# Optimization experiments

Measured on AMD Instinct MI355X. Metric: run time of the kernel, lower is better.

## Reference

```python
import jax, jax.numpy as jnp
import numpy as np

D_MODEL = 2048
NUM_HEADS = 16
NUM_GROUPS = 4
HEAD_DIM = D_MODEL // NUM_HEADS
ROPE_THETA = 10000.0


def apply_rope(x):
    # x: [B, S, H, Dh]; positions = arange(S); interleaved-pair rotary
    B, S, H, Dh = x.shape
    inv_freq = 1.0 / (ROPE_THETA ** (jnp.arange(0, Dh, 2, dtype=jnp.float32) / Dh))  # [Dh/2]
    pos = jnp.arange(S, dtype=jnp.float32)
    ang = pos[:, None] * inv_freq[None, :]            # [S, Dh/2]
    cos = jnp.cos(ang)[None, :, None, :]              # [1, S, 1, Dh/2]
    sin = jnp.sin(ang)[None, :, None, :]
    x1 = x[..., 0::2]
    x2 = x[..., 1::2]
    r1 = x1 * cos - x2 * sin
    r2 = x1 * sin + x2 * cos
    return jnp.stack([r1, r2], axis=-1).reshape(B, S, H, Dh)


def setup_inputs() -> dict:
    key = jax.random.key(0)
    kx, kq, kk, kv, ko = jax.random.split(key, 5)
    B, S = 4, 4096
    x = jax.random.normal(kx, (B, S, D_MODEL), dtype=jnp.float32)
    init = 0.02
    Wq = jax.random.normal(kq, (D_MODEL, D_MODEL), dtype=jnp.float32) * init
    Wk = jax.random.normal(kk, (D_MODEL, D_MODEL), dtype=jnp.float32) * init
    Wv = jax.random.normal(kv, (D_MODEL, D_MODEL), dtype=jnp.float32) * init
    Wo = jax.random.normal(ko, (D_MODEL, D_MODEL), dtype=jnp.float32) * init
    return {"x": x, "Wq": Wq, "Wk": Wk, "Wv": Wv, "Wo": Wo}


def reference(x, Wq, Wk, Wv, Wo):
    B, S, _ = x.shape
    H, G, Dh = NUM_HEADS, NUM_GROUPS, HEAD_DIM
    q = (x @ Wq.T).reshape(B, S, H, Dh)
    k = (x @ Wk.T).reshape(B, S, H, Dh)
    v = (x @ Wv.T).reshape(B, S, H, Dh)
    q = apply_rope(q)
    k = apply_rope(k)
    # GQA head permutation: (B,S,G,H/G,Dh) -> transpose(2,3) -> (B,S,H,Dh)
    q = q.reshape(B, S, G, H // G, Dh).transpose(0, 1, 3, 2, 4).reshape(B, S, H, Dh)
    # NOTE: faithful to source — scores are over the HEAD axis: [B,S,H,H]
    scores = jnp.einsum("bshd,bstd->bsht", q, k) / jnp.sqrt(jnp.asarray(Dh, x.dtype))
    probs = jax.nn.softmax(scores, axis=-1)
    attn = jnp.einsum("bsht,bstd->bshd", probs, v).reshape(B, S, H * Dh)
    return attn @ Wo.T
```

## Files before the change

kernel.cpp:

```cpp
#include <hip/hip_runtime.h>
#include <hip/hip_bf16.h>
#include <stdint.h>


typedef __attribute__((ext_vector_type(8))) short short8;
typedef __attribute__((ext_vector_type(4))) float f32x4;
typedef uint16_t u16;

typedef __attribute__((address_space(1))) const void as1_const_void;
typedef __attribute__((address_space(3))) void as3_void;
#define GLD_LDS16(gp, lp)                                                     \
  __builtin_amdgcn_global_load_lds((as1_const_void*)(gp), (as3_void*)(lp),    \
                                   16, 0, 0)

__device__ __forceinline__ float bf2f(u16 u) {
  uint32_t x = ((uint32_t)u) << 16;
  float f;
  __builtin_memcpy(&f, &x, 4);
  return f;
}
__device__ __forceinline__ u16 f2bf(float f) {
  uint32_t u;
  __builtin_memcpy(&u, &f, 4);
  u += 0x7fffu + ((u >> 16) & 1u);
  return (u16)(u >> 16);
}

__global__ __launch_bounds__(256) void cvt_f32_to_bf16_v4(
    const float* __restrict__ s, u16* __restrict__ d, int n4) {
  int i = blockIdx.x * 256 + threadIdx.x;
  if (i >= n4) return;
  const float4 v = reinterpret_cast<const float4*>(s)[i];
  ushort4 o;
  o.x = f2bf(v.x);
  o.y = f2bf(v.y);
  o.z = f2bf(v.z);
  o.w = f2bf(v.w);
  reinterpret_cast<ushort4*>(d)[i] = o;
}

template <int OUT_F32>
__global__ __launch_bounds__(256, 2) void gemm_bt(
    const u16* __restrict__ A, const u16* __restrict__ B,
    void* __restrict__ Cout, int M, int N, int K) {
  __shared__ u16 sA[128 * 64];
  __shared__ u16 sB[128 * 64];
  const int tid = threadIdx.x;
  const int lane = tid & 63;
  const int wid = tid >> 6;
  const int m0 = blockIdx.y * 128;
  const int n0 = blockIdx.x * 128;
  const int wr = wid >> 1, wc = wid & 1;
  const int lr = lane & 15;
  const int kq = lane >> 4;

  f32x4 acc[4][4];
#pragma unroll
  for (int i = 0; i < 4; ++i)
#pragma unroll
    for (int j = 0; j < 4; ++j) acc[i][j] = {0.f, 0.f, 0.f, 0.f};

  const int nK = K >> 6;
  for (int kt = 0; kt < nK; ++kt) {
    const u16* Ag = A + (size_t)m0 * K + kt * 64;
    const u16* Bg = B + (size_t)n0 * K + kt * 64;
#pragma unroll
    for (int it = 0; it < 4; ++it) {
      const int o = it * 4096 + tid * 16;
      const int row = o >> 7;
      const int lch = ((o >> 4) & 7) ^ (row & 7);
      GLD_LDS16(Ag + (size_t)row * K + lch * 8,
                (char*)sA + it * 4096 + wid * 1024);
    }
#pragma unroll
    for (int it = 0; it < 4; ++it) {
      const int o = it * 4096 + tid * 16;
      const int row = o >> 7;
      const int lch = ((o >> 4) & 7) ^ (row & 7);
      GLD_LDS16(Bg + (size_t)row * K + lch * 8,
                (char*)sB + it * 4096 + wid * 1024);
    }
    __syncthreads();

#pragma unroll
    for (int kk = 0; kk < 2; ++kk) {
      short8 af[4], bfr[4];
#pragma unroll
      for (int f = 0; f < 4; ++f) {
        const int ra = wr * 64 + f * 16 + lr;
        const uint32_t La = (uint32_t)(ra * 128 + kk * 64 + kq * 16);
        af[f] = *reinterpret_cast<const short8*>(
            (const char*)sA + (La ^ (((uint32_t)ra & 7) << 4)));
        const int rb = wc * 64 + f * 16 + lr;
        const uint32_t Lb = (uint32_t)(rb * 128 + kk * 64 + kq * 16);
        bfr[f] = *reinterpret_cast<const short8*>(
            (const char*)sB + (Lb ^ (((uint32_t)rb & 7) << 4)));
      }
#pragma unroll
      for (int i = 0; i < 4; ++i)
#pragma unroll
        for (int j = 0; j < 4; ++j)
          acc[i][j] = __builtin_amdgcn_mfma_f32_16x16x32_bf16(
              af[i], bfr[j], acc[i][j], 0, 0, 0);
    }
    __syncthreads();
  }

  const int rbase = m0 + wr * 64 + (kq << 2);
  const int cbase = n0 + wc * 64 + lr;
  if (OUT_F32) {
    float* C = (float*)Cout;
#pragma unroll
    for (int i = 0; i < 4; ++i)
#pragma unroll
      for (int j = 0; j < 4; ++j)
#pragma unroll
        for (int e = 0; e < 4; ++e)
          C[(size_t)(rbase + i * 16 + e) * N + (cbase + j * 16)] =
              acc[i][j][e];
  } else {
    u16* C = (u16*)Cout;
#pragma unroll
    for (int i = 0; i < 4; ++i)
#pragma unroll
      for (int j = 0; j < 4; ++j)
#pragma unroll
        for (int e = 0; e < 4; ++e)
          C[(size_t)(rbase + i * 16 + e) * N + (cbase + j * 16)] =
              f2bf(acc[i][j][e]);
  }
}

__global__ __launch_bounds__(256) void rope_attn(
    const u16* __restrict__ qkv, u16* __restrict__ attn, int S) {
  __shared__ float cosv[64], sinv[64];
  __shared__ float sq[16][132];
  __shared__ float sk[16][132];
  __shared__ float sp[16][16];
  const int token = blockIdx.x;
  const int s = token & (S - 1);
  const int tid = threadIdx.x;
  const u16* base = qkv + (size_t)token * 6144;

  if (tid < 64) {
    const float inv = powf(10000.0f, -(float)tid * (1.0f / 64.0f));
    float sv, cv;
    sincosf((float)s * inv, &sv, &cv);
    cosv[tid] = cv;
    sinv[tid] = sv;
  }
  __syncthreads();

#pragma unroll
  for (int p = 0; p < 8; ++p) {
    const int idx = p * 256 + tid;
    const int mat = idx >> 10;
    const int rem = idx & 1023;
    const int h = rem >> 6;
    const int i = rem & 63;
    const u16* src = base + mat * 2048 + h * 128 + 2 * i;
    const float x1 = bf2f(src[0]);
    const float x2 = bf2f(src[1]);
    const float c = cosv[i], sn = sinv[i];
    float* dst = mat ? sk[h] : sq[h];
    dst[2 * i] = x1 * c - x2 * sn;
    dst[2 * i + 1] = x1 * sn + x2 * c;
  }
  __syncthreads();

  {
    const int h = tid >> 4;
    const int t = tid & 15;
    const int hp = ((h & 3) << 2) | (h >> 2);
    float sc = 0.f;
#pragma unroll
    for (int d = 0; d < 128; ++d) sc += sq[hp][d] * sk[t][d];
    sc *= 0.08838834764831845f;
    float mx = sc;
#pragma unroll
    for (int o = 8; o; o >>= 1) mx = fmaxf(mx, __shfl_xor(mx, o, 16));
    const float e = __expf(sc - mx);
    float sum = e;
#pragma unroll
    for (int o = 8; o; o >>= 1) sum += __shfl_xor(sum, o, 16);
    sp[h][t] = e / sum;
  }
  __syncthreads();

  {
    const int h = tid >> 4;
    const int d0 = (tid & 15) * 8;
    const u16* vb = base + 4096;
    float o[8] = {0.f, 0.f, 0.f, 0.f, 0.f, 0.f, 0.f, 0.f};
#pragma unroll
    for (int t = 0; t < 16; ++t) {
      const float pr = sp[h][t];
      const short8 vv = *reinterpret_cast<const short8*>(vb + t * 128 + d0);
#pragma unroll
      for (int e = 0; e < 8; ++e) o[e] += pr * bf2f((u16)vv[e]);
    }
    short8 ov;
#pragma unroll
    for (int e = 0; e < 8; ++e) ov[e] = (short)f2bf(o[e]);
    *reinterpret_cast<short8*>(attn + (size_t)token * 2048 + h * 128 + d0) =
        ov;
  }
}

extern "C" void kernel_launch(void* const* d_in, const int* in_sizes, int n_in,
                              void* d_out, int out_size, void* d_ws,
                              size_t ws_size, hipStream_t stream) {
  (void)in_sizes;
  (void)n_in;
  (void)out_size;
  (void)ws_size;
  const float* x = (const float*)d_in[0];
  const float* Wq = (const float*)d_in[1];
  const float* Wk = (const float*)d_in[2];
  const float* Wv = (const float*)d_in[3];
  const float* Wo = (const float*)d_in[4];
  float* out = (float*)d_out;

  const int B = 4, S = 4096, D = 2048;
  const int M = B * S;

  char* ws = (char*)d_ws;
  u16* xb = (u16*)ws;
  u16* wqkv = (u16*)(ws + (size_t)M * D * 2);
  u16* wo = (u16*)((char*)wqkv + (size_t)3 * D * D * 2);
  u16* qkv = (u16*)((char*)wo + (size_t)D * D * 2);

  cvt_f32_to_bf16_v4<<<(M * D / 4 + 255) / 256, 256, 0, stream>>>(x, xb,
                                                                  M * D / 4);
  const int w4 = D * D / 4;
  cvt_f32_to_bf16_v4<<<(w4 + 255) / 256, 256, 0, stream>>>(Wq, wqkv, w4);
  cvt_f32_to_bf16_v4<<<(w4 + 255) / 256, 256, 0, stream>>>(
      Wk, wqkv + (size_t)D * D, w4);
  cvt_f32_to_bf16_v4<<<(w4 + 255) / 256, 256, 0, stream>>>(
      Wv, wqkv + (size_t)2 * D * D, w4);
  cvt_f32_to_bf16_v4<<<(w4 + 255) / 256, 256, 0, stream>>>(Wo, wo, w4);

  gemm_bt<0><<<dim3(3 * D / 128, M / 128), 256, 0, stream>>>(xb, wqkv, qkv, M,
                                                             3 * D, D);
  rope_attn<<<M, 256, 0, stream>>>(qkv, xb, S);
  gemm_bt<1><<<dim3(D / 128, M / 128), 256, 0, stream>>>(xb, wo, out, M, D, D);
}
```

Before: 668.2 us.

## Double-buffer GEMM LDS tiles to overlap global loads with MFMA compute

Adds a second LDS buffer for the A and B tiles in the shared GEMM kernel. The next K tile is issued with global_load_lds before the current one is consumed, and a partial vmcnt wait plus a raw s_barrier replaces __syncthreads, so memory latency can be hidden behind the MFMAs. LDS use doubles to 64KB per block, which may limit the intended two blocks per CU. The hand-written waitcnt and barrier assembly carries correctness risk if the compiler reorders LDS reads.

```diff
diff --git a/kernel.cpp b/kernel.cpp
--- a/kernel.cpp
+++ b/kernel.cpp
@@ -12,6 +12,9 @@
 #define GLD_LDS16(gp, lp)                                                     \
   __builtin_amdgcn_global_load_lds((as1_const_void*)(gp), (as3_void*)(lp),    \
                                    16, 0, 0)
+
+#define BAR() asm volatile("s_barrier" ::: "memory")
+#define VMCNT(n) asm volatile("s_waitcnt vmcnt(" #n ")" ::: "memory")
 
 __device__ __forceinline__ float bf2f(u16 u) {
   uint32_t x = ((uint32_t)u) << 16;
@@ -43,8 +46,8 @@
 __global__ __launch_bounds__(256, 2) void gemm_bt(
     const u16* __restrict__ A, const u16* __restrict__ B,
     void* __restrict__ Cout, int M, int N, int K) {
-  __shared__ u16 sA[128 * 64];
-  __shared__ u16 sB[128 * 64];
+  __shared__ u16 sA[2][128 * 64];
+  __shared__ u16 sB[2][128 * 64];
   const int tid = threadIdx.x;
   const int lane = tid & 63;
   const int wid = tid >> 6;
@@ -61,27 +64,36 @@
     for (int j = 0; j < 4; ++j) acc[i][j] = {0.f, 0.f, 0.f, 0.f};
 
   const int nK = K >> 6;
-  for (int kt = 0; kt < nK; ++kt) {
-    const u16* Ag = A + (size_t)m0 * K + kt * 64;
-    const u16* Bg = B + (size_t)n0 * K + kt * 64;
+
+  auto stage = [&](int buf, int kt) {
+    const u16* Ag = A + (size_t)m0 * K + (size_t)kt * 64;
+    const u16* Bg = B + (size_t)n0 * K + (size_t)kt * 64;
 #pragma unroll
     for (int it = 0; it < 4; ++it) {
       const int o = it * 4096 + tid * 16;
       const int row = o >> 7;
       const int lch = ((o >> 4) & 7) ^ (row & 7);
       GLD_LDS16(Ag + (size_t)row * K + lch * 8,
-                (char*)sA + it * 4096 + wid * 1024);
-    }
-#pragma unroll
-    for (int it = 0; it < 4; ++it) {
-      const int o = it * 4096 + tid * 16;
-      const int row = o >> 7;
-      const int lch = ((o >> 4) & 7) ^ (row & 7);
+                (char*)sA[buf] + it * 4096 + wid * 1024);
       GLD_LDS16(Bg + (size_t)row * K + lch * 8,
-                (char*)sB + it * 4096 + wid * 1024);
-    }
-    __syncthreads();
-
+                (char*)sB[buf] + it * 4096 + wid * 1024);
+    }
+  };
+
+  stage(0, 0);
+
+  int cur = 0;
+  for (int kt = 0; kt < nK; ++kt, cur ^= 1) {
+    if (kt + 1 < nK) {
+      stage(cur ^ 1, kt + 1);
+      VMCNT(8);
+    } else {
+      VMCNT(0);
+    }
+    BAR();
+
+    const u16* sAc = sA[cur];
+    const u16* sBc = sB[cur];
 #pragma unroll
     for (int kk = 0; kk < 2; ++kk) {
       short8 af[4], bfr[4];
@@ -90,11 +102,11 @@
         const int ra = wr * 64 + f * 16 + lr;
         const uint32_t La = (uint32_t)(ra * 128 + kk * 64 + kq * 16);
         af[f] = *reinterpret_cast<const short8*>(
-            (const char*)sA + (La ^ (((uint32_t)ra & 7) << 4)));
+            (const char*)sAc + (La ^ (((uint32_t)ra & 7) << 4)));
         const int rb = wc * 64 + f * 16 + lr;
         const uint32_t Lb = (uint32_t)(rb * 128 + kk * 64 + kq * 16);
         bfr[f] = *reinterpret_cast<const short8*>(
-            (const char*)sB + (Lb ^ (((uint32_t)rb & 7) << 4)));
+            (const char*)sBc + (Lb ^ (((uint32_t)rb & 7) << 4)));
       }
 #pragma unroll
       for (int i = 0; i < 4; ++i)
@@ -103,7 +115,7 @@
           acc[i][j] = __builtin_amdgcn_mfma_f32_16x16x32_bf16(
               af[i], bfr[j], acc[i][j], 0, 0, 0);
     }
-    __syncthreads();
+    BAR();
   }
 
   const int rbase = m0 + wr * 64 + (kq << 2);
```

Result: slower. 789.5 us (+18.2%).

## Rewrite per-token head attention as one-wave-per-token MFMA kernel, merge weight conversions

Applied to the files above, without the earlier changes.

The rope+head-attention kernel now handles one token per wavefront, four per block. RoPE runs in registers, the 16x16 head score matrix comes from MFMA instructions, softmax uses wave shuffles, and V and the probabilities are staged in per-wave LDS. This drops the block-wide barriers and the scalar fp32 dot products of the old one-token-per-block kernel. The four weight conversion launches are merged into one kernel, which relies on wo sitting directly after wqkv in the workspace. Q and K are rounded to bf16 after RoPE, adding some precision loss, and the LDS handoff uses only an lgkmcnt wait with no barrier, which is safe only because each wave touches its own slice.

```diff
diff --git a/kernel.cpp b/kernel.cpp
--- a/kernel.cpp
+++ b/kernel.cpp
@@ -37,6 +37,23 @@
   o.z = f2bf(v.z);
   o.w = f2bf(v.w);
   reinterpret_cast<ushort4*>(d)[i] = o;
+}
+
+__global__ __launch_bounds__(256) void cvt_w4(
+    const float* __restrict__ w0, const float* __restrict__ w1,
+    const float* __restrict__ w2, const float* __restrict__ w3,
+    u16* __restrict__ dst) {
+  const int i = blockIdx.x * 256 + threadIdx.x;
+  const int m = i >> 20;
+  const int r = i & ((1 << 20) - 1);
+  const float* src = (m == 0) ? w0 : (m == 1) ? w1 : (m == 2) ? w2 : w3;
+  const float4 v = reinterpret_cast<const float4*>(src)[r];
+  ushort4 o;
+  o.x = f2bf(v.x);
+  o.y = f2bf(v.y);
+  o.z = f2bf(v.z);
+  o.w = f2bf(v.w);
+  reinterpret_cast<ushort4*>(dst)[i] = o;
 }
 
 template <int OUT_F32>
@@ -131,79 +148,108 @@
   }
 }
 
-__global__ __launch_bounds__(256) void rope_attn(
+__global__ __launch_bounds__(256) void rope_attn2(
     const u16* __restrict__ qkv, u16* __restrict__ attn, int S) {
-  __shared__ float cosv[64], sinv[64];
-  __shared__ float sq[16][132];
-  __shared__ float sk[16][132];
-  __shared__ float sp[16][16];
-  const int token = blockIdx.x;
-  const int s = token & (S - 1);
+  __shared__ u16 vld[4][16][136];
+  __shared__ float pld[4][16][17];
   const int tid = threadIdx.x;
+  const int l = tid & 63;
+  const int w = tid >> 6;
+  const int token = blockIdx.x * 4 + w;
+  const int pos = token & (S - 1);
   const u16* base = qkv + (size_t)token * 6144;
 
-  if (tid < 64) {
-    const float inv = powf(10000.0f, -(float)tid * (1.0f / 64.0f));
-    float sv, cv;
-    sincosf((float)s * inv, &sv, &cv);
-    cosv[tid] = cv;
-    sinv[tid] = sv;
-  }
-  __syncthreads();
-
-#pragma unroll
-  for (int p = 0; p < 8; ++p) {
-    const int idx = p * 256 + tid;
-    const int mat = idx >> 10;
-    const int rem = idx & 1023;
-    const int h = rem >> 6;
-    const int i = rem & 63;
-    const u16* src = base + mat * 2048 + h * 128 + 2 * i;
-    const float x1 = bf2f(src[0]);
-    const float x2 = bf2f(src[1]);
-    const float c = cosv[i], sn = sinv[i];
-    float* dst = mat ? sk[h] : sq[h];
-    dst[2 * i] = x1 * c - x2 * sn;
-    dst[2 * i + 1] = x1 * sn + x2 * c;
-  }
-  __syncthreads();
-
+  const int vt = l >> 2, vd0 = (l & 3) * 32;
+  short8 vreg[4];
   {
-    const int h = tid >> 4;
-    const int t = tid & 15;
-    const int hp = ((h & 3) << 2) | (h >> 2);
-    float sc = 0.f;
-#pragma unroll
-    for (int d = 0; d < 128; ++d) sc += sq[hp][d] * sk[t][d];
-    sc *= 0.08838834764831845f;
-    float mx = sc;
-#pragma unroll
-    for (int o = 8; o; o >>= 1) mx = fmaxf(mx, __shfl_xor(mx, o, 16));
-    const float e = __expf(sc - mx);
-    float sum = e;
-#pragma unroll
-    for (int o = 8; o; o >>= 1) sum += __shfl_xor(sum, o, 16);
-    sp[h][t] = e / sum;
-  }
-  __syncthreads();
-
-  {
-    const int h = tid >> 4;
-    const int d0 = (tid & 15) * 8;
-    const u16* vb = base + 4096;
-    float o[8] = {0.f, 0.f, 0.f, 0.f, 0.f, 0.f, 0.f, 0.f};
-#pragma unroll
-    for (int t = 0; t < 16; ++t) {
-      const float pr = sp[h][t];
-      const short8 vv = *reinterpret_cast<const short8*>(vb + t * 128 + d0);
-#pragma unroll
-      for (int e = 0; e < 8; ++e) o[e] += pr * bf2f((u16)vv[e]);
-    }
+    const u16* vsrc = base + 4096 + vt * 128 + vd0;
+#pragma unroll
+    for (int c = 0; c < 4; ++c)
+      vreg[c] = *reinterpret_cast<const short8*>(vsrc + c * 8);
+  }
+
+  const int hq = (((l & 15) & 3) << 2) | ((l & 15) >> 2);
+  const u16* qsrc = base + hq * 128;
+  const u16* ksrc = base + 2048 + (l & 15) * 128;
+  short8 aq[4], ak[4];
+#pragma unroll
+  for (int kk = 0; kk < 4; ++kk) {
+    const int d0 = kk * 32 + ((l >> 4) << 3);
+    const short8 qv = *reinterpret_cast<const short8*>(qsrc + d0);
+    const short8 kv = *reinterpret_cast<const short8*>(ksrc + d0);
+    short8 qo, ko;
+#pragma unroll
+    for (int j = 0; j < 4; ++j) {
+      const int i = (d0 >> 1) + j;
+      const float invf = __expf(-0.14391156831212787f * (float)i);
+      float sv, cv;
+      sincosf((float)pos * invf, &sv, &cv);
+      const float q1 = bf2f((u16)qv[2 * j]), q2 = bf2f((u16)qv[2 * j + 1]);
+      const float k1 = bf2f((u16)kv[2 * j]), k2 = bf2f((u16)kv[2 * j + 1]);
+      qo[2 * j] = (short)f2bf(q1 * cv - q2 * sv);
+      qo[2 * j + 1] = (short)f2bf(q1 * sv + q2 * cv);
+      ko[2 * j] = (short)f2bf(k1 * cv - k2 * sv);
+      ko[2 * j + 1] = (short)f2bf(k1 * sv + k2 * cv);
+    }
+    aq[kk] = qo;
+    ak[kk] = ko;
+  }
+
+  f32x4 accS = {0.f, 0.f, 0.f, 0.f};
+#pragma unroll
+  for (int kk = 0; kk < 4; ++kk)
+    accS = __builtin_amdgcn_mfma_f32_16x16x32_bf16(ak[kk], aq[kk], accS, 0, 0,
+                                                   0);
+
+  float p[4];
+  float mx = -3.4e38f;
+#pragma unroll
+  for (int e = 0; e < 4; ++e) {
+    p[e] = accS[e] * 0.08838834764831845f;
+    mx = fmaxf(mx, p[e]);
+  }
+  mx = fmaxf(mx, __shfl_xor(mx, 16));
+  mx = fmaxf(mx, __shfl_xor(mx, 32));
+  float sum = 0.f;
+#pragma unroll
+  for (int e = 0; e < 4; ++e) {
+    p[e] = __expf(p[e] - mx);
+    sum += p[e];
+  }
+  sum += __shfl_xor(sum, 16);
+  sum += __shfl_xor(sum, 32);
+  const float rs = 1.0f / sum;
+
+#pragma unroll
+  for (int c = 0; c < 4; ++c)
+    *reinterpret_cast<short8*>(&vld[w][vt][vd0 + c * 8]) = vreg[c];
+#pragma unroll
+  for (int e = 0; e < 4; ++e)
+    pld[w][((l >> 4) << 2) + e][l & 15] = p[e] * rs;
+  asm volatile("s_waitcnt lgkmcnt(0)" ::: "memory");
+
+  const int ph = l >> 2, pd0 = (l & 3) * 32;
+  float o[32];
+#pragma unroll
+  for (int e = 0; e < 32; ++e) o[e] = 0.f;
+  for (int t = 0; t < 16; ++t) {
+    const float pv = pld[w][t][ph];
+#pragma unroll
+    for (int c = 0; c < 4; ++c) {
+      const short8 vv =
+          *reinterpret_cast<const short8*>(&vld[w][t][pd0 + c * 8]);
+#pragma unroll
+      for (int e2 = 0; e2 < 8; ++e2) o[c * 8 + e2] += pv * bf2f((u16)vv[e2]);
+    }
+  }
+
+  u16* dst = attn + (size_t)token * 2048 + ph * 128 + pd0;
+#pragma unroll
+  for (int c = 0; c < 4; ++c) {
     short8 ov;
 #pragma unroll
-    for (int e = 0; e < 8; ++e) ov[e] = (short)f2bf(o[e]);
-    *reinterpret_cast<short8*>(attn + (size_t)token * 2048 + h * 128 + d0) =
-        ov;
+    for (int e2 = 0; e2 < 8; ++e2) ov[e2] = (short)f2bf(o[c * 8 + e2]);
+    *reinterpret_cast<short8*>(dst + c * 8) = ov;
   }
 }
 
@@ -232,16 +278,10 @@
 
   cvt_f32_to_bf16_v4<<<(M * D / 4 + 255) / 256, 256, 0, stream>>>(x, xb,
                                                                   M * D / 4);
-  const int w4 = D * D / 4;
-  cvt_f32_to_bf16_v4<<<(w4 + 255) / 256, 256, 0, stream>>>(Wq, wqkv, w4);
-  cvt_f32_to_bf16_v4<<<(w4 + 255) / 256, 256, 0, stream>>>(
-      Wk, wqkv + (size_t)D * D, w4);
-  cvt_f32_to_bf16_v4<<<(w4 + 255) / 256, 256, 0, stream>>>(
-      Wv, wqkv + (size_t)2 * D * D, w4);
-  cvt_f32_to_bf16_v4<<<(w4 + 255) / 256, 256, 0, stream>>>(Wo, wo, w4);
+  cvt_w4<<<4 * (D * D / 4) / 256, 256, 0, stream>>>(Wq, Wk, Wv, Wo, wqkv);
 
   gemm_bt<0><<<dim3(3 * D / 128, M / 128), 256, 0, stream>>>(xb, wqkv, qkv, M,
                                                              3 * D, D);
-  rope_attn<<<M, 256, 0, stream>>>(qkv, xb, S);
+  rope_attn2<<<M / 4, 256, 0, stream>>>(qkv, xb, S);
   gemm_bt<1><<<dim3(D / 128, M / 128), 256, 0, stream>>>(xb, wo, out, M, D, D);
 }
```

New measurement: 651.1 us. 2.5% less time.
